# Performance work log

Measured on AMD Instinct MI355X. Metric: run time of the kernel, lower is better.

Reference implementation:

```python
import jax, jax.numpy as jnp
import numpy as np

NUM_ENT = 40000
NUM_REL = 100
EMBED_DIM = 256
FEAT_DIM = 768
BATCH = 32
SEQ_LEN = 3
MASK_POS = 2
EPS = 1e-12


def setup_inputs() -> dict:
    key = jax.random.key(0)
    k1, k2, k3, k4 = jax.random.split(key, 4)
    ent_pkl = jax.random.normal(k1, (NUM_ENT, FEAT_DIM), dtype=jnp.float32)
    other_emb = jax.random.normal(k2, (NUM_ENT + NUM_REL + 3 - NUM_ENT, EMBED_DIM), dtype=jnp.float32)
    proj_W = jax.random.normal(k3, (EMBED_DIM, FEAT_DIM), dtype=jnp.float32) * (1.0 / np.sqrt(FEAT_DIM))
    batch_input_ids = jax.random.randint(k4, (BATCH, SEQ_LEN), 0, NUM_ENT + NUM_REL + 3, dtype=jnp.int64)
    return {
        "ent_pkl": ent_pkl,
        "other_emb": other_emb,
        "proj_W": proj_W,
        "batch_input_ids": batch_input_ids,
        "batch_mask_position": MASK_POS,
    }


def reference(ent_pkl, other_emb, proj_W, batch_input_ids, batch_mask_position):
    # unity embeddings: [other[0], proj(ent_pkl), other[1:]] -> [num_ent+num_rel+3, d]
    ent_proj = ent_pkl @ proj_W.T  # Linear(feat_dim, embed_dim, bias=False)
    unity = jnp.concatenate([other_emb[:1], ent_proj, other_emb[1:]], axis=0)

    mp = int(batch_mask_position)
    # drop the masked slot, keep up to 3 tokens total -> [B, 2]
    query_input = jnp.concatenate(
        [batch_input_ids[:, :mp], batch_input_ids[:, mp + 1:3]], axis=1)
    query_emb = unity[query_input]  # [B, 2, d]
    # F.normalize(dim=-1): x / max(||x||_2, eps)
    norm = jnp.sqrt(jnp.sum(query_emb * query_emb, axis=-1, keepdims=True))
    query_emb = query_emb / jnp.maximum(norm, EPS)
    query_sum = jnp.sum(query_emb, axis=1)  # [B, d]

    E_embed = unity[:NUM_ENT + 1]  # [num_ent+1, d]
    # broadcast L1 distance: [B, num_ent+1]
    score = -jnp.sum(jnp.abs(query_sum[:, None, :] - E_embed[None, :, :]), axis=-1)
    return score
```

## Files before the change

kernel.cpp:

```cpp
#include <hip/hip_runtime.h>
#include <hip/hip_bf16.h>
#include <stdint.h>

#define NE 40000
#define FD 768
#define ED 256
#define NB 32
#define OUTC (NE + 1)

typedef __bf16 bf16x8 __attribute__((ext_vector_type(8)));
typedef float f32x4 __attribute__((ext_vector_type(4)));
typedef float f32x16 __attribute__((ext_vector_type(16)));
typedef _Float16 f16x2 __attribute__((ext_vector_type(2)));
typedef _Float16 f16x4 __attribute__((ext_vector_type(4)));

#define WS_QS 0
#define WS_N01 (32 * 1024)
#define WS_WB (96 * 1024)

__device__ __forceinline__ f16x2 pabs2(f16x2 d) {
    union { f16x2 h; unsigned u; } v; v.h = d; v.u &= 0x7FFF7FFFu; return v.h;
}

__global__ __launch_bounds__(256) void prep_kernel(
    const float* __restrict__ ent_pkl, const float* __restrict__ W,
    const int* __restrict__ ids, const int* __restrict__ mpos,
    __bf16* __restrict__ Wf, float* __restrict__ n01_raw)
{
    const int bid = blockIdx.x;
    const int t = threadIdx.x;

    if (bid < 96) {
        const int f = bid * 256 + t;
        const int w = f / 3072;
        const int r = f - w * 3072;
        const int g = r >> 6;
        const int l = r & 63;
        const float* src = W + (size_t)(32 * w + (l & 31)) * FD + g * 16 + (l >> 5) * 8;
        float4 a = *(const float4*)src;
        float4 b = *(const float4*)(src + 4);
        bf16x8 v;
        v[0] = (__bf16)a.x; v[1] = (__bf16)a.y; v[2] = (__bf16)a.z; v[3] = (__bf16)a.w;
        v[4] = (__bf16)b.x; v[5] = (__bf16)b.y; v[6] = (__bf16)b.z; v[7] = (__bf16)b.w;
        *(bf16x8*)(Wf + (size_t)f * 8) = v;
        return;
    }

    __shared__ float row[FD];
    const int slot = bid - 96;
    const int b = slot >> 1, s = slot & 1;
    const int mp = mpos[0];
    const int col = (s < mp) ? s : s + 1;
    const bool wide = (ids[1] == 0 && ids[3] == 0 && ids[5] == 0);
    const int flat = b * 3 + col;
    const int idx = wide ? ids[flat * 2] : ids[flat];
    if (!(idx >= 1 && idx <= NE)) return;

    const float* src = ent_pkl + (size_t)(idx - 1) * FD;
    for (int k = t; k < FD; k += 256) row[k] = src[k];
    __syncthreads();

    const float4* w4 = (const float4*)(W + (size_t)t * FD);
    const float4* r4 = (const float4*)row;
    float a0 = 0.f, a1 = 0.f, a2 = 0.f, a3 = 0.f;
#pragma unroll 2
    for (int k4 = 0; k4 < FD / 4; k4 += 4) {
        float4 w0 = w4[k4 + 0], r0 = r4[k4 + 0];
        float4 w1 = w4[k4 + 1], r1 = r4[k4 + 1];
        float4 w2 = w4[k4 + 2], r2 = r4[k4 + 2];
        float4 w3 = w4[k4 + 3], r3 = r4[k4 + 3];
        a0 += w0.x * r0.x + w0.y * r0.y + w0.z * r0.z + w0.w * r0.w;
        a1 += w1.x * r1.x + w1.y * r1.y + w1.z * r1.z + w1.w * r1.w;
        a2 += w2.x * r2.x + w2.y * r2.y + w2.z * r2.z + w2.w * r2.w;
        a3 += w3.x * r3.x + w3.y * r3.y + w3.z * r3.z + w3.w * r3.w;
    }
    n01_raw[slot * ED + t] = (a0 + a1) + (a2 + a3);
}

__global__ __launch_bounds__(256) void qsum_kernel(
    const float* __restrict__ other_emb, const float* __restrict__ n01_raw,
    const int* __restrict__ ids, const int* __restrict__ mpos,
    _Float16* __restrict__ qh, float* __restrict__ out)
{
    __shared__ float red[4];
    __shared__ float nshare;
    const int b = blockIdx.x, t = threadIdx.x;
    const int mp = mpos[0];
    const bool wide = (ids[1] == 0 && ids[3] == 0 && ids[5] == 0);

    float q = 0.f;
#pragma unroll
    for (int s = 0; s < 2; ++s) {
        const int col = (s < mp) ? s : s + 1;
        const int flat = b * 3 + col;
        const int idx = wide ? ids[flat * 2] : ids[flat];
        float v;
        if (idx >= 1 && idx <= NE) v = n01_raw[(b * 2 + s) * ED + t];
        else if (idx == 0) v = other_emb[t];
        else v = other_emb[(size_t)(idx - NE) * ED + t];

        float ss = v * v;
#pragma unroll
        for (int o = 32; o > 0; o >>= 1) ss += __shfl_down(ss, o, 64);
        if ((t & 63) == 0) red[t >> 6] = ss;
        __syncthreads();
        if (t == 0) nshare = fmaxf(sqrtf(red[0] + red[1] + red[2] + red[3]), 1e-12f);
        __syncthreads();
        q += v / nshare;
        __syncthreads();
    }
    qh[b * ED + t] = (_Float16)q;

    float d = fabsf(q - other_emb[t]);
#pragma unroll
    for (int o = 32; o > 0; o >>= 1) d += __shfl_down(d, o, 64);
    if ((t & 63) == 0) red[t >> 6] = d;
    __syncthreads();
    if (t == 0) out[(size_t)b * OUTC] = -(red[0] + red[1] + red[2] + red[3]);
}

#define SP 260

__global__ __launch_bounds__(512, 6) void gemm_score_kernel(
    const float* __restrict__ ent_pkl, const __bf16* __restrict__ Wf,
    const _Float16* __restrict__ qh, float* __restrict__ out)
{
    __shared__ __align__(16) unsigned char smem[49152];
    __bf16* Asm = (__bf16*)smem;
    _Float16* Sb = (_Float16*)smem;

    const int t = threadIdx.x;
    const int l = t & 63;
    const int w = t >> 6;
    const int m31 = l & 31;
    const int dh = l >> 5;
    const int e0 = blockIdx.x * 64;

    f32x16 acc0, acc1;
#pragma unroll
    for (int i = 0; i < 16; ++i) { acc0[i] = 0.f; acc1[i] = 0.f; }

    const int srow = t >> 3;
    const int sseg = t & 7;
    const int ssw = srow & 7;
    const __bf16* bp = Wf + (size_t)w * 24576 + (size_t)l * 8;
    const __bf16* arow0 = Asm + m31 * 384;
    const __bf16* arow1 = Asm + (32 + m31) * 384;
    const int asw = m31 & 7;

#pragma unroll
    for (int h = 0; h < 2; ++h) {
        __syncthreads();
        {
            const float* ap = ent_pkl + (size_t)(e0 + srow) * FD + h * 384 + sseg * 48;
            const f32x4* ap4 = (const f32x4*)ap;
            __bf16* dst = Asm + srow * 384;
#pragma unroll
            for (int j = 0; j < 6; ++j) {
                f32x4 x = __builtin_nontemporal_load(ap4 + 2 * j);
                f32x4 y = __builtin_nontemporal_load(ap4 + 2 * j + 1);
                bf16x8 v;
                v[0] = (__bf16)x[0]; v[1] = (__bf16)x[1]; v[2] = (__bf16)x[2]; v[3] = (__bf16)x[3];
                v[4] = (__bf16)y[0]; v[5] = (__bf16)y[1]; v[6] = (__bf16)y[2]; v[7] = (__bf16)y[3];
                *(bf16x8*)(dst + ((sseg * 6 + j) ^ ssw) * 8) = v;
            }
        }
        __syncthreads();
#pragma unroll 4
        for (int c = 0; c < 24; ++c) {
            bf16x8 bv = *(const bf16x8*)(bp + (size_t)(h * 24 + c) * 512);
            const int oct = (2 * c + dh) ^ asw;
            bf16x8 a0 = *(const bf16x8*)(arow0 + oct * 8);
            bf16x8 a1 = *(const bf16x8*)(arow1 + oct * 8);
            acc0 = __builtin_amdgcn_mfma_f32_32x32x16_bf16(a0, bv, acc0, 0, 0, 0);
            acc1 = __builtin_amdgcn_mfma_f32_32x32x16_bf16(a1, bv, acc1, 0, 0, 0);
        }
    }

    __syncthreads();
#pragma unroll
    for (int r = 0; r < 16; ++r) {
        const int erow = (r & 3) + 8 * (r >> 2) + 4 * dh;
        Sb[erow * SP + 32 * w + m31] = (_Float16)acc0[r];
        Sb[(32 + erow) * SP + 32 * w + m31] = (_Float16)acc1[r];
    }
    __syncthreads();

    const int wu = __builtin_amdgcn_readfirstlane(w);
    const f16x4* q0 = (const f16x4*)(qh + (size_t)(4 * wu + 0) * ED);
    const f16x4* q1 = (const f16x4*)(qh + (size_t)(4 * wu + 1) * ED);
    const f16x4* q2 = (const f16x4*)(qh + (size_t)(4 * wu + 2) * ED);
    const f16x4* q3 = (const f16x4*)(qh + (size_t)(4 * wu + 3) * ED);
    const f16x4* xrow = (const f16x4*)(Sb + (size_t)l * SP);

    float s0 = 0.f, s1 = 0.f, s2 = 0.f, s3 = 0.f;
    for (int cb = 0; cb < 8; ++cb) {
        f16x2 t0 = {0, 0}, t1 = {0, 0}, t2 = {0, 0}, t3 = {0, 0};
#pragma unroll
        for (int ci = 0; ci < 8; ++ci) {
            const int c = cb * 8 + ci;
            f16x4 xv = xrow[c];
            f16x2 xlo = __builtin_shufflevector(xv, xv, 0, 1);
            f16x2 xhi = __builtin_shufflevector(xv, xv, 2, 3);
            f16x4 qa = q0[c], qb = q1[c], qc = q2[c], qd = q3[c];
            t0 = t0 + pabs2(__builtin_shufflevector(qa, qa, 0, 1) - xlo);
            t0 = t0 + pabs2(__builtin_shufflevector(qa, qa, 2, 3) - xhi);
            t1 = t1 + pabs2(__builtin_shufflevector(qb, qb, 0, 1) - xlo);
            t1 = t1 + pabs2(__builtin_shufflevector(qb, qb, 2, 3) - xhi);
            t2 = t2 + pabs2(__builtin_shufflevector(qc, qc, 0, 1) - xlo);
            t2 = t2 + pabs2(__builtin_shufflevector(qc, qc, 2, 3) - xhi);
            t3 = t3 + pabs2(__builtin_shufflevector(qd, qd, 0, 1) - xlo);
            t3 = t3 + pabs2(__builtin_shufflevector(qd, qd, 2, 3) - xhi);
        }
        s0 += (float)t0[0] + (float)t0[1];
        s1 += (float)t1[0] + (float)t1[1];
        s2 += (float)t2[0] + (float)t2[1];
        s3 += (float)t3[0] + (float)t3[1];
    }
    float* ob = out + 1 + e0 + l;
    __builtin_nontemporal_store(-s0, ob + (size_t)(4 * wu + 0) * OUTC);
    __builtin_nontemporal_store(-s1, ob + (size_t)(4 * wu + 1) * OUTC);
    __builtin_nontemporal_store(-s2, ob + (size_t)(4 * wu + 2) * OUTC);
    __builtin_nontemporal_store(-s3, ob + (size_t)(4 * wu + 3) * OUTC);
}

extern "C" void kernel_launch(void* const* d_in, const int* in_sizes, int n_in,
                              void* d_out, int out_size, void* d_ws, size_t ws_size,
                              hipStream_t stream) {
    const float* ent_pkl = (const float*)d_in[0];
    const float* other_emb = (const float*)d_in[1];
    const float* proj_W = (const float*)d_in[2];
    const int* ids = (const int*)d_in[3];
    const int* mpos = (const int*)d_in[4];
    float* out = (float*)d_out;

    _Float16* qh = (_Float16*)((char*)d_ws + WS_QS);
    float* n01_raw = (float*)((char*)d_ws + WS_N01);
    __bf16* Wf = (__bf16*)((char*)d_ws + WS_WB);

    prep_kernel<<<160, 256, 0, stream>>>(ent_pkl, proj_W, ids, mpos, Wf, n01_raw);
    qsum_kernel<<<NB, 256, 0, stream>>>(other_emb, n01_raw, ids, mpos, qh, out);
    gemm_score_kernel<<<NE / 64, 512, 0, stream>>>(ent_pkl, Wf, qh, out);
}
```

Before: 278.4 us.

## Stream ent_pkl tiles to LDS via global_load_lds and convert to bf16 at use

The GEMM kernel now moves fp32 ent_pkl tiles straight into LDS with global_load_lds across four K quarters, instead of loading them into registers, converting to bf16 and writing them back to LDS. The bf16 conversion moves into the MFMA inner loop. The score tile uses an XOR-swizzled layout in place of padding, and the query vectors are staged in LDS. The prep kernel also changes: the W reformat uses coalesced row reads, and the small projection is split across four times as many blocks with wave-level shuffle reductions. This trades register round-trips for extra LDS traffic and conversion work in the inner loop, and adds more barriers per K quarter.

```diff
diff --git a/kernel.cpp b/kernel.cpp
--- a/kernel.cpp
+++ b/kernel.cpp
@@ -22,32 +22,34 @@
     union { f16x2 h; unsigned u; } v; v.h = d; v.u &= 0x7FFF7FFFu; return v.h;
 }
 
+__device__ __forceinline__ void gload16(const void* g, void* l) {
+    __builtin_amdgcn_global_load_lds(
+        (const __attribute__((address_space(1))) unsigned int*)g,
+        (__attribute__((address_space(3))) unsigned int*)l, 16, 0, 0);
+}
+
 __global__ __launch_bounds__(256) void prep_kernel(
     const float* __restrict__ ent_pkl, const float* __restrict__ W,
     const int* __restrict__ ids, const int* __restrict__ mpos,
     __bf16* __restrict__ Wf, float* __restrict__ n01_raw)
 {
+    __shared__ f32x4 xs4[FD / 4];
     const int bid = blockIdx.x;
     const int t = threadIdx.x;
 
-    if (bid < 96) {
-        const int f = bid * 256 + t;
-        const int w = f / 3072;
-        const int r = f - w * 3072;
-        const int g = r >> 6;
-        const int l = r & 63;
-        const float* src = W + (size_t)(32 * w + (l & 31)) * FD + g * 16 + (l >> 5) * 8;
-        float4 a = *(const float4*)src;
-        float4 b = *(const float4*)(src + 4);
-        bf16x8 v;
-        v[0] = (__bf16)a.x; v[1] = (__bf16)a.y; v[2] = (__bf16)a.z; v[3] = (__bf16)a.w;
-        v[4] = (__bf16)b.x; v[5] = (__bf16)b.y; v[6] = (__bf16)b.z; v[7] = (__bf16)b.w;
-        *(bf16x8*)(Wf + (size_t)f * 8) = v;
+    if (bid < 192) {
+        const int i = bid * 1024 + t * 4;
+        const int r = i / FD, c = i - r * FD;
+        float4 v = *(const float4*)(W + i);
+        __bf16 o[4] = {(__bf16)v.x, (__bf16)v.y, (__bf16)v.z, (__bf16)v.w};
+        const int f = ((r >> 5) * 48 + (c >> 4)) * 64 + (r & 31) + ((c >> 3) & 1) * 32;
+        *(ushort4*)(Wf + (size_t)f * 8 + (c & 7)) = *(const ushort4*)o;
         return;
     }
 
-    __shared__ float row[FD];
-    const int slot = bid - 96;
+    const int sub = bid - 192;
+    const int slot = sub >> 2;
+    const int oq = sub & 3;
     const int b = slot >> 1, s = slot & 1;
     const int mp = mpos[0];
     const int col = (s < mp) ? s : s + 1;
@@ -56,25 +58,24 @@
     const int idx = wide ? ids[flat * 2] : ids[flat];
     if (!(idx >= 1 && idx <= NE)) return;
 
-    const float* src = ent_pkl + (size_t)(idx - 1) * FD;
-    for (int k = t; k < FD; k += 256) row[k] = src[k];
-    __syncthreads();
-
-    const float4* w4 = (const float4*)(W + (size_t)t * FD);
-    const float4* r4 = (const float4*)row;
-    float a0 = 0.f, a1 = 0.f, a2 = 0.f, a3 = 0.f;
+    if (t < FD / 4) xs4[t] = ((const f32x4*)(ent_pkl + (size_t)(idx - 1) * FD))[t];
+    __syncthreads();
+
+    const int l = t & 63, wv = t >> 6;
+    const f32x4 x0 = xs4[l], x1 = xs4[l + 64], x2 = xs4[l + 128];
+    const int obase = oq * 64 + wv * 16;
 #pragma unroll 2
-    for (int k4 = 0; k4 < FD / 4; k4 += 4) {
-        float4 w0 = w4[k4 + 0], r0 = r4[k4 + 0];
-        float4 w1 = w4[k4 + 1], r1 = r4[k4 + 1];
-        float4 w2 = w4[k4 + 2], r2 = r4[k4 + 2];
-        float4 w3 = w4[k4 + 3], r3 = r4[k4 + 3];
-        a0 += w0.x * r0.x + w0.y * r0.y + w0.z * r0.z + w0.w * r0.w;
-        a1 += w1.x * r1.x + w1.y * r1.y + w1.z * r1.z + w1.w * r1.w;
-        a2 += w2.x * r2.x + w2.y * r2.y + w2.z * r2.z + w2.w * r2.w;
-        a3 += w3.x * r3.x + w3.y * r3.y + w3.z * r3.z + w3.w * r3.w;
-    }
-    n01_raw[slot * ED + t] = (a0 + a1) + (a2 + a3);
+    for (int i = 0; i < 16; ++i) {
+        const int o = obase + i;
+        const f32x4* wr = (const f32x4*)(W + (size_t)o * FD);
+        f32x4 w0 = wr[l], w1 = wr[l + 64], w2 = wr[l + 128];
+        float p = w0[0] * x0[0] + w0[1] * x0[1] + w0[2] * x0[2] + w0[3] * x0[3]
+                + w1[0] * x1[0] + w1[1] * x1[1] + w1[2] * x1[2] + w1[3] * x1[3]
+                + w2[0] * x2[0] + w2[1] * x2[1] + w2[2] * x2[2] + w2[3] * x2[3];
+#pragma unroll
+        for (int off = 32; off; off >>= 1) p += __shfl_xor(p, off, 64);
+        if (l == 0) n01_raw[slot * ED + o] = p;
+    }
 }
 
 __global__ __launch_bounds__(256) void qsum_kernel(
@@ -119,15 +120,16 @@
     if (t == 0) out[(size_t)b * OUTC] = -(red[0] + red[1] + red[2] + red[3]);
 }
 
-#define SP 260
+#define SP 256
 
 __global__ __launch_bounds__(512, 6) void gemm_score_kernel(
     const float* __restrict__ ent_pkl, const __bf16* __restrict__ Wf,
     const _Float16* __restrict__ qh, float* __restrict__ out)
 {
     __shared__ __align__(16) unsigned char smem[49152];
-    __bf16* Asm = (__bf16*)smem;
+    float* Af = (float*)smem;
     _Float16* Sb = (_Float16*)smem;
+    _Float16* qL = (_Float16*)(smem + 32768);
 
     const int t = threadIdx.x;
     const int l = t & 63;
@@ -140,58 +142,73 @@
 #pragma unroll
     for (int i = 0; i < 16; ++i) { acc0[i] = 0.f; acc1[i] = 0.f; }
 
-    const int srow = t >> 3;
-    const int sseg = t & 7;
-    const int ssw = srow & 7;
+    int srow[6], slc[6];
+#pragma unroll
+    for (int j = 0; j < 6; ++j) {
+        const int p = j * 512 + t;
+        const int r = p / 48;
+        srow[j] = r;
+        slc[j] = (p - r * 48) ^ (r & 7);
+    }
+
     const __bf16* bp = Wf + (size_t)w * 24576 + (size_t)l * 8;
-    const __bf16* arow0 = Asm + m31 * 384;
-    const __bf16* arow1 = Asm + (32 + m31) * 384;
-    const int asw = m31 & 7;
-
-#pragma unroll
-    for (int h = 0; h < 2; ++h) {
-        __syncthreads();
-        {
-            const float* ap = ent_pkl + (size_t)(e0 + srow) * FD + h * 384 + sseg * 48;
-            const f32x4* ap4 = (const f32x4*)ap;
-            __bf16* dst = Asm + srow * 384;
-#pragma unroll
-            for (int j = 0; j < 6; ++j) {
-                f32x4 x = __builtin_nontemporal_load(ap4 + 2 * j);
-                f32x4 y = __builtin_nontemporal_load(ap4 + 2 * j + 1);
-                bf16x8 v;
-                v[0] = (__bf16)x[0]; v[1] = (__bf16)x[1]; v[2] = (__bf16)x[2]; v[3] = (__bf16)x[3];
-                v[4] = (__bf16)y[0]; v[5] = (__bf16)y[1]; v[6] = (__bf16)y[2]; v[7] = (__bf16)y[3];
-                *(bf16x8*)(dst + ((sseg * 6 + j) ^ ssw) * 8) = v;
-            }
+    const int sw = m31 & 7;
+    const float* a0base = Af + m31 * 192;
+    const float* a1base = Af + (32 + m31) * 192;
+
+    for (int q = 0; q < 4; ++q) {
+        __syncthreads();
+#pragma unroll
+        for (int j = 0; j < 6; ++j) {
+            gload16(ent_pkl + (size_t)(e0 + srow[j]) * FD + q * 192 + slc[j] * 4,
+                    (float*)smem + (size_t)(j * 512 + t) * 4);
         }
         __syncthreads();
+        const __bf16* bq = bp + (size_t)q * 12 * 512;
 #pragma unroll 4
-        for (int c = 0; c < 24; ++c) {
-            bf16x8 bv = *(const bf16x8*)(bp + (size_t)(h * 24 + c) * 512);
-            const int oct = (2 * c + dh) ^ asw;
-            bf16x8 a0 = *(const bf16x8*)(arow0 + oct * 8);
-            bf16x8 a1 = *(const bf16x8*)(arow1 + oct * 8);
+        for (int c = 0; c < 12; ++c) {
+            bf16x8 bv = *(const bf16x8*)(bq + c * 512);
+            const int u0 = 4 * c + 2 * dh;
+            const int p0 = (u0 ^ sw) * 4, p1 = ((u0 + 1) ^ sw) * 4;
+            f32x4 lo0 = *(const f32x4*)(a0base + p0);
+            f32x4 hi0 = *(const f32x4*)(a0base + p1);
+            f32x4 lo1 = *(const f32x4*)(a1base + p0);
+            f32x4 hi1 = *(const f32x4*)(a1base + p1);
+            bf16x8 a0, a1;
+            a0[0] = (__bf16)lo0[0]; a0[1] = (__bf16)lo0[1]; a0[2] = (__bf16)lo0[2]; a0[3] = (__bf16)lo0[3];
+            a0[4] = (__bf16)hi0[0]; a0[5] = (__bf16)hi0[1]; a0[6] = (__bf16)hi0[2]; a0[7] = (__bf16)hi0[3];
+            a1[0] = (__bf16)lo1[0]; a1[1] = (__bf16)lo1[1]; a1[2] = (__bf16)lo1[2]; a1[3] = (__bf16)lo1[3];
+            a1[4] = (__bf16)hi1[0]; a1[5] = (__bf16)hi1[1]; a1[6] = (__bf16)hi1[2]; a1[7] = (__bf16)hi1[3];
             acc0 = __builtin_amdgcn_mfma_f32_32x32x16_bf16(a0, bv, acc0, 0, 0, 0);
             acc1 = __builtin_amdgcn_mfma_f32_32x32x16_bf16(a1, bv, acc1, 0, 0, 0);
         }
     }
 
     __syncthreads();
+    const int colg = 8 * w + (m31 >> 2);
+    const int csub = m31 & 3;
 #pragma unroll
     for (int r = 0; r < 16; ++r) {
         const int erow = (r & 3) + 8 * (r >> 2) + 4 * dh;
-        Sb[erow * SP + 32 * w + m31] = (_Float16)acc0[r];
-        Sb[(32 + erow) * SP + 32 * w + m31] = (_Float16)acc1[r];
+        const int ph = (((colg ^ (erow & 15)) << 2) | csub);
+        Sb[erow * SP + ph] = (_Float16)acc0[r];
+        Sb[(32 + erow) * SP + ph] = (_Float16)acc1[r];
+    }
+    {
+        const uint4* qsrc = (const uint4*)qh;
+        uint4* qdst = (uint4*)qL;
+        qdst[t] = qsrc[t];
+        qdst[t + 512] = qsrc[t + 512];
     }
     __syncthreads();
 
     const int wu = __builtin_amdgcn_readfirstlane(w);
-    const f16x4* q0 = (const f16x4*)(qh + (size_t)(4 * wu + 0) * ED);
-    const f16x4* q1 = (const f16x4*)(qh + (size_t)(4 * wu + 1) * ED);
-    const f16x4* q2 = (const f16x4*)(qh + (size_t)(4 * wu + 2) * ED);
-    const f16x4* q3 = (const f16x4*)(qh + (size_t)(4 * wu + 3) * ED);
-    const f16x4* xrow = (const f16x4*)(Sb + (size_t)l * SP);
+    const f16x4* q0 = (const f16x4*)(qL + (size_t)(4 * wu + 0) * ED);
+    const f16x4* q1 = (const f16x4*)(qL + (size_t)(4 * wu + 1) * ED);
+    const f16x4* q2 = (const f16x4*)(qL + (size_t)(4 * wu + 2) * ED);
+    const f16x4* q3 = (const f16x4*)(qL + (size_t)(4 * wu + 3) * ED);
+    const int swl = l & 15;
+    const _Float16* xbase = Sb + (size_t)l * SP;
 
     float s0 = 0.f, s1 = 0.f, s2 = 0.f, s3 = 0.f;
     for (int cb = 0; cb < 8; ++cb) {
@@ -199,7 +216,7 @@
 #pragma unroll
         for (int ci = 0; ci < 8; ++ci) {
             const int c = cb * 8 + ci;
-            f16x4 xv = xrow[c];
+            f16x4 xv = *(const f16x4*)(xbase + ((c ^ swl) << 2));
             f16x2 xlo = __builtin_shufflevector(xv, xv, 0, 1);
             f16x2 xhi = __builtin_shufflevector(xv, xv, 2, 3);
             f16x4 qa = q0[c], qb = q1[c], qc = q2[c], qd = q3[c];
@@ -238,7 +255,7 @@
     float* n01_raw = (float*)((char*)d_ws + WS_N01);
     __bf16* Wf = (__bf16*)((char*)d_ws + WS_WB);
 
-    prep_kernel<<<160, 256, 0, stream>>>(ent_pkl, proj_W, ids, mpos, Wf, n01_raw);
+    prep_kernel<<<448, 256, 0, stream>>>(ent_pkl, proj_W, ids, mpos, Wf, n01_raw);
     qsum_kernel<<<NB, 256, 0, stream>>>(other_emb, n01_raw, ids, mpos, qh, out);
     gemm_score_kernel<<<NE / 64, 512, 0, stream>>>(ent_pkl, Wf, qh, out);
 }
```

Measured after the change: 245.4 us. 11.8% less time.
